# Optimization experiments

Hardware: AMD Instinct MI355X
Metric: run time of the kernel (lower is better)

Reference implementation:

```python
import jax, jax.numpy as jnp
import numpy as np

N, C, H, W = 32, 256, 64, 64
K = 1024  # embed_size


def setup_inputs() -> dict:
    key = jax.random.key(0)
    k1, k2 = jax.random.split(key)
    x = jax.random.normal(k1, (N, C, H, W), dtype=jnp.float32)
    embed = jax.random.normal(k2, (K, C), dtype=jnp.float32)  # codebook buffer
    return {"x": x, "embed": embed}


def reference(x, embed):
    n, c, h, w = x.shape
    # [N,C,H,W] -> [N*H*W, C]
    flat = jnp.transpose(x, (0, 2, 3, 1)).reshape(-1, c)
    # squared euclidean distance; sqrt omitted since argmin is invariant
    d = (
        jnp.sum(flat * flat, axis=-1, keepdims=True)
        - 2.0 * flat @ embed.T
        + jnp.sum(embed * embed, axis=-1)
    )  # [N*H*W, K]
    embed_idx = jnp.argmin(d, axis=1).reshape(n, h, w)
    quantize = embed[embed_idx]  # [N,H,W,C]
    quantize = jnp.transpose(quantize, (0, 3, 1, 2))  # [N,C,H,W]
    diff = jnp.mean((jax.lax.stop_gradient(quantize) - x) ** 2)
    quantize = x + jax.lax.stop_gradient(quantize - x)  # straight-through
    return quantize, embed_idx, diff
```

## Files before the change

kernel.cpp:

```cpp
#include <hip/hip_runtime.h>

#define NB    32
#define CDIM  256
#define HWSZ  4096
#define NPOS  (NB*HWSZ)
#define KCODES 1024
#define QELEMS ((size_t)NB*CDIM*HWSZ)
#define IDX_OFF QELEMS
#define DIFF_OFF (QELEMS + NPOS)
#define EBYTES (32*32768)
#define E2F_OFF (EBYTES/4)

#define AOFF  0
#define BOFF  65536
#define X2P   131072
#define X2T   133120
#define MVOFF 133376
#define MIOFF 135424
#define LDSSZ 137472

typedef _Float16       f16x8  __attribute__((ext_vector_type(8)));
typedef float          f32x16 __attribute__((ext_vector_type(16)));
typedef unsigned short u16x8  __attribute__((ext_vector_type(8)));

static __device__ inline unsigned short f2h(float f) {
    _Float16 h = (_Float16)f;
    return __builtin_bit_cast(unsigned short, h);
}

__global__ __launch_bounds__(64) void vq_prep_embed(const float* __restrict__ embed,
                                                    float* __restrict__ out) {
    const int k = blockIdx.x;
    const int lane = threadIdx.x;
    const float4 v = *reinterpret_cast<const float4*>(embed + (size_t)k * CDIM + lane * 4);

    unsigned char* __restrict__ ebuf = (unsigned char*)out;

    _Float16 h0 = (_Float16)v.x, h1 = (_Float16)v.y, h2 = (_Float16)v.z, h3 = (_Float16)v.w;
    ushort4 hv = { __builtin_bit_cast(unsigned short, h0), __builtin_bit_cast(unsigned short, h1),
                   __builtin_bit_cast(unsigned short, h2), __builtin_bit_cast(unsigned short, h3) };
    ushort4 lv = { f2h((v.x - (float)h0) * 64.0f), f2h((v.y - (float)h1) * 64.0f),
                   f2h((v.z - (float)h2) * 64.0f), f2h((v.w - (float)h3) * 64.0f) };

    const int c0   = lane * 4;
    const int tile = c0 >> 4;
    const int kh   = (c0 >> 3) & 1;
    const int sub  = c0 & 7;
    const size_t byte = (size_t)tile * 32768 + (size_t)kh * 16384 + (size_t)k * 16 + sub * 2;
    *reinterpret_cast<ushort4*>(ebuf + byte)              = hv;
    *reinterpret_cast<ushort4*>(ebuf + byte + 16 * 32768) = lv;

    float s = v.x * v.x + v.y * v.y + v.z * v.z + v.w * v.w;
    #pragma unroll
    for (int m = 1; m < 64; m <<= 1) s += __shfl_xor(s, m, 64);
    if (lane == 0) out[E2F_OFF + k] = s;
    if (k == 0 && lane == 0) out[DIFF_OFF] = 0.0f;
}

__global__ __launch_bounds__(512, 2) void vq_stage1(const float* __restrict__ x,
                                                    float* __restrict__ out) {
    __shared__ __align__(16) unsigned char lds[LDSSZ];

    const unsigned char* __restrict__ ebuf = (const unsigned char*)out;
    const float* __restrict__ e2buf = out + E2F_OFF;
    float* __restrict__ idx_out = out + IDX_OFF;

    const int t     = threadIdx.x;
    const int lane  = t & 63;
    const int col32 = lane & 31;
    const int hi    = lane >> 5;
    const int widx  = t >> 6;

    const int pos0 = blockIdx.x * 64;
    const int n    = pos0 >> 12;
    const int hw0  = pos0 & 4095;
    const float* __restrict__ xbase = x + (size_t)n * (CDIM * HWSZ) + hw0;

    {
        const int i = t & 63;
        const int g = t >> 6;
        float x2p = 0.f;
        #pragma unroll
        for (int j = 0; j < 4; ++j) {
            const int c0 = g * 32 + j * 8;
            u16x8 hv, lv;
            #pragma unroll
            for (int q = 0; q < 8; ++q) {
                float vv = xbase[(size_t)(c0 + q) * HWSZ + i];
                x2p = fmaf(vv, vv, x2p);
                _Float16 hh = (_Float16)vv;
                hv[q] = __builtin_bit_cast(unsigned short, hh);
                lv[q] = f2h((vv - (float)hh) * 64.0f);
            }
            const int a  = c0 >> 4;
            const int kh = (c0 >> 3) & 1;
            const int byte = a * 2048 + kh * 1024 + i * 16;
            *reinterpret_cast<u16x8*>(lds + byte)         = hv;
            *reinterpret_cast<u16x8*>(lds + byte + 32768) = lv;
        }
        ((float*)(lds + X2P))[g * 64 + i] = x2p;
    }

    auto stage = [&](int tile, int buf) {
        const unsigned char* src = ebuf + (size_t)tile * 32768;
        unsigned char* dst = lds + BOFF + buf * 32768;
        #pragma unroll
        for (int ii = 0; ii < 4; ++ii) {
            const int chunk = (widx * 4 + ii) * 1024;
            __builtin_amdgcn_global_load_lds(
                (const __attribute__((address_space(1))) unsigned int*)(src + chunk + lane * 16),
                (__attribute__((address_space(3))) unsigned int*)(dst + chunk),
                16, 0, 0);
        }
    };

    stage(0, 0);
    __syncthreads();

    if (t < 64) {
        const float* p = (const float*)(lds + X2P);
        float s = 0.f;
        #pragma unroll
        for (int g = 0; g < 8; ++g) s += p[g * 64 + t];
        ((float*)(lds + X2T))[t] = s;
    }

    f32x16 acc[2][4];
    #pragma unroll
    for (int ra = 0; ra < 2; ++ra)
        #pragma unroll
        for (int cb = 0; cb < 4; ++cb)
            #pragma unroll
            for (int r = 0; r < 16; ++r) acc[ra][cb][r] = 0.f;

    const int aoff_lane = hi * 1024 + col32 * 16;
    const int boff_lane = hi * 16384 + (widx * 128 + col32) * 16;

    int buf = 0;
    for (int kq = 0; kq < 48; ++kq) {
        const int nb = kq + 1;
        if (nb < 48) stage(nb < 32 ? nb : nb - 32, buf ^ 1);

        const int a = (kq < 16) ? kq : kq - 16;
        const unsigned char* ab = lds + a * 2048;
        const unsigned char* bb = lds + BOFF + buf * 32768;

        f16x8 av[2], bv[4];
        #pragma unroll
        for (int ra = 0; ra < 2; ++ra)
            av[ra] = *reinterpret_cast<const f16x8*>(ab + aoff_lane + ra * 512);
        #pragma unroll
        for (int cb = 0; cb < 4; ++cb)
            bv[cb] = *reinterpret_cast<const f16x8*>(bb + boff_lane + cb * 512);

        if (kq >= 16 && kq < 32) {
            #pragma unroll
            for (int ra = 0; ra < 2; ++ra) av[ra] *= (_Float16)0.015625f;
        } else if (kq >= 32) {
            #pragma unroll
            for (int cb = 0; cb < 4; ++cb) bv[cb] *= (_Float16)0.015625f;
        }

        __builtin_amdgcn_s_setprio(1);
        #pragma unroll
        for (int ra = 0; ra < 2; ++ra)
            #pragma unroll
            for (int cb = 0; cb < 4; ++cb)
                acc[ra][cb] = __builtin_amdgcn_mfma_f32_32x32x16_f16(
                    av[ra], bv[cb], acc[ra][cb], 0, 0, 0);
        __builtin_amdgcn_s_setprio(0);

        __syncthreads();
        buf ^= 1;
    }

    const float* x2t = (const float*)(lds + X2T);
    float e2v[4];
    #pragma unroll
    for (int cb = 0; cb < 4; ++cb)
        e2v[cb] = e2buf[widx * 128 + cb * 32 + col32];

    float* mv = (float*)(lds + MVOFF);
    int*   mi = (int*)(lds + MIOFF);

    #pragma unroll
    for (int ra = 0; ra < 2; ++ra) {
        #pragma unroll
        for (int reg = 0; reg < 16; ++reg) {
            const int pos = ra * 32 + (reg & 3) + 8 * (reg >> 2) + 4 * hi;
            const float x2 = x2t[pos];
            float bv_ = 3.4e38f;
            int   bi_ = 0;
            #pragma unroll
            for (int cb = 0; cb < 4; ++cb) {
                const int code = widx * 128 + cb * 32 + col32;
                const float s = (x2 - 2.0f * acc[ra][cb][reg]) + e2v[cb];
                if (s < bv_) { bv_ = s; bi_ = code; }
            }
            #pragma unroll
            for (int m = 1; m < 32; m <<= 1) {
                float ov = __shfl_xor(bv_, m, 64);
                int   oi = __shfl_xor(bi_, m, 64);
                if (ov < bv_ || (ov == bv_ && oi < bi_)) { bv_ = ov; bi_ = oi; }
            }
            if (col32 == 0) {
                mv[widx * 64 + pos] = bv_;
                mi[widx * 64 + pos] = bi_;
            }
        }
    }

    __syncthreads();
    if (t < 64) {
        float bv_ = mv[t];
        int   bi_ = mi[t];
        #pragma unroll
        for (int w = 1; w < 8; ++w) {
            const float ov = mv[w * 64 + t];
            const int   oi = mi[w * 64 + t];
            if (ov < bv_ || (ov == bv_ && oi < bi_)) { bv_ = ov; bi_ = oi; }
        }
        idx_out[pos0 + t] = (float)bi_;
        float d = bv_;
        #pragma unroll
        for (int m = 1; m < 64; m <<= 1) d += __shfl_xor(d, m, 64);
        if (t == 0) atomicAdd(out + DIFF_OFF, d * (1.0f / 33554432.0f));
    }
}

__global__ __launch_bounds__(256) void vq_gather_kernel(const float* __restrict__ embed,
                                                        float* __restrict__ out) {
    const int tid = threadIdx.x;
    const int p = blockIdx.x * 256 + tid;
    const int n = p >> 12;
    const int hw = p & 4095;
    const int idx = (int)out[IDX_OFF + p];
    const float4* __restrict__ erow4 = reinterpret_cast<const float4*>(embed + (size_t)idx * CDIM);
    float* __restrict__ op = out + (size_t)n * (CDIM * HWSZ) + hw;

    #pragma unroll 8
    for (int c4 = 0; c4 < 64; ++c4) {
        const float4 e = erow4[c4];
        op[(size_t)(c4 * 4 + 0) * HWSZ] = e.x;
        op[(size_t)(c4 * 4 + 1) * HWSZ] = e.y;
        op[(size_t)(c4 * 4 + 2) * HWSZ] = e.z;
        op[(size_t)(c4 * 4 + 3) * HWSZ] = e.w;
    }
}

extern "C" void kernel_launch(void* const* d_in, const int* in_sizes, int n_in,
                              void* d_out, int out_size, void* d_ws, size_t ws_size,
                              hipStream_t stream) {
    const float* x = (const float*)d_in[0];
    const float* embed = (const float*)d_in[1];
    float* out = (float*)d_out;

    vq_prep_embed<<<KCODES, 64, 0, stream>>>(embed, out);
    vq_stage1<<<NPOS / 64, 512, 0, stream>>>(x, out);
    vq_gather_kernel<<<NPOS / 256, 256, 0, stream>>>(embed, out);
}
```

Baseline: 431.9 us.

## Reuse each staged codebook tile for hi and lo A parts in one pass

The K-loop shrinks from 48 iterations to 32. Each codebook tile is staged once, and while it is resident it is used for both the high and low fp16 split of the activations, where before several tiles were restaged. This cuts global-to-LDS traffic and barrier count. The per-iteration __syncthreads is replaced with an explicit vmcnt wait plus raw s_barrier pairs, so prefetch stays in flight across the barrier. The manual waitcnt accounting is fragile, and the final prefetch wraps to tile 0 and loads data that is never used.

Result: slower. 1.277 ms (+195.7%).

```diff
diff --git a/kernel.cpp b/kernel.cpp
--- a/kernel.cpp
+++ b/kernel.cpp
@@ -11,7 +11,6 @@
 #define EBYTES (32*32768)
 #define E2F_OFF (EBYTES/4)
 
-#define AOFF  0
 #define BOFF  65536
 #define X2P   131072
 #define X2T   133120
@@ -114,8 +113,8 @@
         }
     };
 
+    __syncthreads();
     stage(0, 0);
-    __syncthreads();
 
     if (t < 64) {
         const float* p = (const float*)(lds + X2P);
@@ -136,42 +135,64 @@
     const int aoff_lane = hi * 1024 + col32 * 16;
     const int boff_lane = hi * 16384 + (widx * 128 + col32) * 16;
 
-    int buf = 0;
-    for (int kq = 0; kq < 48; ++kq) {
-        const int nb = kq + 1;
-        if (nb < 48) stage(nb < 32 ? nb : nb - 32, buf ^ 1);
-
-        const int a = (kq < 16) ? kq : kq - 16;
-        const unsigned char* ab = lds + a * 2048;
-        const unsigned char* bb = lds + BOFF + buf * 32768;
-
-        f16x8 av[2], bv[4];
-        #pragma unroll
-        for (int ra = 0; ra < 2; ++ra)
-            av[ra] = *reinterpret_cast<const f16x8*>(ab + aoff_lane + ra * 512);
-        #pragma unroll
-        for (int cb = 0; cb < 4; ++cb)
-            bv[cb] = *reinterpret_cast<const f16x8*>(bb + boff_lane + cb * 512);
-
-        if (kq >= 16 && kq < 32) {
-            #pragma unroll
-            for (int ra = 0; ra < 2; ++ra) av[ra] *= (_Float16)0.015625f;
-        } else if (kq >= 32) {
+    for (int kt = 0; kt < 32; ++kt) {
+        stage((kt + 1) & 31, (kt + 1) & 1);
+        asm volatile("s_waitcnt vmcnt(4)" ::: "memory");
+        __builtin_amdgcn_s_barrier();
+
+        const unsigned char* bb = lds + BOFF + (kt & 1) * 32768;
+
+        if (kt < 16) {
+            const unsigned char* ab = lds + kt * 2048;
+            f16x8 ah[2], al[2], bv[4];
+            #pragma unroll
+            for (int ra = 0; ra < 2; ++ra) {
+                ah[ra] = *reinterpret_cast<const f16x8*>(ab + aoff_lane + ra * 512);
+                al[ra] = *reinterpret_cast<const f16x8*>(ab + 32768 + aoff_lane + ra * 512);
+            }
+            #pragma unroll
+            for (int cb = 0; cb < 4; ++cb)
+                bv[cb] = *reinterpret_cast<const f16x8*>(bb + boff_lane + cb * 512);
+
+            __builtin_amdgcn_s_setprio(1);
+            #pragma unroll
+            for (int ra = 0; ra < 2; ++ra)
+                #pragma unroll
+                for (int cb = 0; cb < 4; ++cb)
+                    acc[ra][cb] = __builtin_amdgcn_mfma_f32_32x32x16_f16(
+                        ah[ra], bv[cb], acc[ra][cb], 0, 0, 0);
             #pragma unroll
             for (int cb = 0; cb < 4; ++cb) bv[cb] *= (_Float16)0.015625f;
-        }
-
-        __builtin_amdgcn_s_setprio(1);
-        #pragma unroll
-        for (int ra = 0; ra < 2; ++ra)
+            #pragma unroll
+            for (int ra = 0; ra < 2; ++ra)
+                #pragma unroll
+                for (int cb = 0; cb < 4; ++cb)
+                    acc[ra][cb] = __builtin_amdgcn_mfma_f32_32x32x16_f16(
+                        al[ra], bv[cb], acc[ra][cb], 0, 0, 0);
+            __builtin_amdgcn_s_setprio(0);
+        } else {
+            const unsigned char* ab = lds + (kt - 16) * 2048;
+            f16x8 ah[2], bv[4];
+            #pragma unroll
+            for (int ra = 0; ra < 2; ++ra) {
+                ah[ra] = *reinterpret_cast<const f16x8*>(ab + aoff_lane + ra * 512);
+                ah[ra] *= (_Float16)0.015625f;
+            }
             #pragma unroll
             for (int cb = 0; cb < 4; ++cb)
-                acc[ra][cb] = __builtin_amdgcn_mfma_f32_32x32x16_f16(
-                    av[ra], bv[cb], acc[ra][cb], 0, 0, 0);
-        __builtin_amdgcn_s_setprio(0);
-
-        __syncthreads();
-        buf ^= 1;
+                bv[cb] = *reinterpret_cast<const f16x8*>(bb + boff_lane + cb * 512);
+
+            __builtin_amdgcn_s_setprio(1);
+            #pragma unroll
+            for (int ra = 0; ra < 2; ++ra)
+                #pragma unroll
+                for (int cb = 0; cb < 4; ++cb)
+                    acc[ra][cb] = __builtin_amdgcn_mfma_f32_32x32x16_f16(
+                        ah[ra], bv[cb], acc[ra][cb], 0, 0, 0);
+            __builtin_amdgcn_s_setprio(0);
+        }
+
+        __builtin_amdgcn_s_barrier();
     }
 
     const float* x2t = (const float*)(lds + X2T);
```

## Load codebook fragments straight from global memory instead of LDS double buffering

Applied to the files above, without the earlier changes.

The per-iteration global_load_lds staging of codebook tiles into double-buffered LDS is removed. Each wave now reads its own 128-code B fragments directly from global memory (L2) into registers, using a re-laid-out prepped codebook where each code row is 32 contiguous bytes. Because each wave only ever consumed its own slice of the staged tile, the staging added no reuse. Dropping it removes the per-iteration __syncthreads and roughly halves LDS use, which may allow more resident blocks per CU. In exchange, global-memory latency is exposed in the MFMA loop, covered only by a 2x unroll and whatever occupancy is gained.

After: 413.3 us. 4.3% less time.

```diff
diff --git a/kernel.cpp b/kernel.cpp
--- a/kernel.cpp
+++ b/kernel.cpp
@@ -11,13 +11,11 @@
 #define EBYTES (32*32768)
 #define E2F_OFF (EBYTES/4)
 
-#define AOFF  0
-#define BOFF  65536
-#define X2P   131072
-#define X2T   133120
-#define MVOFF 133376
-#define MIOFF 135424
-#define LDSSZ 137472
+#define X2P   65536
+#define X2T   67584
+#define MVOFF 67840
+#define MIOFF 69888
+#define LDSSZ 71936
 
 typedef _Float16       f16x8  __attribute__((ext_vector_type(8)));
 typedef float          f32x16 __attribute__((ext_vector_type(16)));
@@ -42,11 +40,11 @@
     ushort4 lv = { f2h((v.x - (float)h0) * 64.0f), f2h((v.y - (float)h1) * 64.0f),
                    f2h((v.z - (float)h2) * 64.0f), f2h((v.w - (float)h3) * 64.0f) };
 
-    const int c0   = lane * 4;
-    const int tile = c0 >> 4;
-    const int kh   = (c0 >> 3) & 1;
-    const int sub  = c0 & 7;
-    const size_t byte = (size_t)tile * 32768 + (size_t)kh * 16384 + (size_t)k * 16 + sub * 2;
+    const int c0  = lane * 4;
+    const int r   = c0 >> 4;
+    const int hi  = (c0 >> 3) & 1;
+    const int sub = c0 & 7;
+    const size_t byte = (size_t)r * 32768 + (size_t)k * 32 + hi * 16 + sub * 2;
     *reinterpret_cast<ushort4*>(ebuf + byte)              = hv;
     *reinterpret_cast<ushort4*>(ebuf + byte + 16 * 32768) = lv;
 
@@ -57,8 +55,8 @@
     if (k == 0 && lane == 0) out[DIFF_OFF] = 0.0f;
 }
 
-__global__ __launch_bounds__(512, 2) void vq_stage1(const float* __restrict__ x,
-                                                    float* __restrict__ out) {
+__global__ __launch_bounds__(512) void vq_stage1(const float* __restrict__ x,
+                                                 float* __restrict__ out) {
     __shared__ __align__(16) unsigned char lds[LDSSZ];
 
     const unsigned char* __restrict__ ebuf = (const unsigned char*)out;
@@ -92,29 +90,14 @@
                 hv[q] = __builtin_bit_cast(unsigned short, hh);
                 lv[q] = f2h((vv - (float)hh) * 64.0f);
             }
-            const int a  = c0 >> 4;
+            const int kc = c0 >> 4;
             const int kh = (c0 >> 3) & 1;
-            const int byte = a * 2048 + kh * 1024 + i * 16;
+            const int byte = kc * 2048 + kh * 1024 + i * 16;
             *reinterpret_cast<u16x8*>(lds + byte)         = hv;
             *reinterpret_cast<u16x8*>(lds + byte + 32768) = lv;
         }
         ((float*)(lds + X2P))[g * 64 + i] = x2p;
     }
-
-    auto stage = [&](int tile, int buf) {
-        const unsigned char* src = ebuf + (size_t)tile * 32768;
-        unsigned char* dst = lds + BOFF + buf * 32768;
-        #pragma unroll
-        for (int ii = 0; ii < 4; ++ii) {
-            const int chunk = (widx * 4 + ii) * 1024;
-            __builtin_amdgcn_global_load_lds(
-                (const __attribute__((address_space(1))) unsigned int*)(src + chunk + lane * 16),
-                (__attribute__((address_space(3))) unsigned int*)(dst + chunk),
-                16, 0, 0);
-        }
-    };
-
-    stage(0, 0);
     __syncthreads();
 
     if (t < 64) {
@@ -124,6 +107,7 @@
         for (int g = 0; g < 8; ++g) s += p[g * 64 + t];
         ((float*)(lds + X2T))[t] = s;
     }
+    __syncthreads();
 
     f32x16 acc[2][4];
     #pragma unroll
@@ -133,45 +117,44 @@
             #pragma unroll
             for (int r = 0; r < 16; ++r) acc[ra][cb][r] = 0.f;
 
-    const int aoff_lane = hi * 1024 + col32 * 16;
-    const int boff_lane = hi * 16384 + (widx * 128 + col32) * 16;
-
-    int buf = 0;
+    const int aoff = hi * 1024 + col32 * 16;
+    const unsigned char* __restrict__ bbase =
+        ebuf + (size_t)widx * 4096 + (size_t)col32 * 32 + (size_t)hi * 16;
+
+    #pragma unroll 2
     for (int kq = 0; kq < 48; ++kq) {
-        const int nb = kq + 1;
-        if (nb < 48) stage(nb < 32 ? nb : nb - 32, buf ^ 1);
-
-        const int a = (kq < 16) ? kq : kq - 16;
-        const unsigned char* ab = lds + a * 2048;
-        const unsigned char* bb = lds + BOFF + buf * 32768;
-
-        f16x8 av[2], bv[4];
-        #pragma unroll
-        for (int ra = 0; ra < 2; ++ra)
-            av[ra] = *reinterpret_cast<const f16x8*>(ab + aoff_lane + ra * 512);
-        #pragma unroll
-        for (int cb = 0; cb < 4; ++cb)
-            bv[cb] = *reinterpret_cast<const f16x8*>(bb + boff_lane + cb * 512);
-
-        if (kq >= 16 && kq < 32) {
-            #pragma unroll
-            for (int ra = 0; ra < 2; ++ra) av[ra] *= (_Float16)0.015625f;
-        } else if (kq >= 32) {
-            #pragma unroll
-            for (int cb = 0; cb < 4; ++cb) bv[cb] *= (_Float16)0.015625f;
+        const int seg = kq >> 4;
+        const int r   = (kq < 32) ? kq : (kq - 32);
+        const unsigned char* ab = lds + (kq & 15) * 2048 + ((seg == 2) ? 32768 : 0);
+        const unsigned char* bp = bbase + (size_t)r * 32768;
+
+        f16x8 a0 = *reinterpret_cast<const f16x8*>(ab + aoff);
+        f16x8 a1 = *reinterpret_cast<const f16x8*>(ab + aoff + 512);
+        f16x8 b0 = *reinterpret_cast<const f16x8*>(bp);
+        f16x8 b1 = *reinterpret_cast<const f16x8*>(bp + 1024);
+        f16x8 b2 = *reinterpret_cast<const f16x8*>(bp + 2048);
+        f16x8 b3 = *reinterpret_cast<const f16x8*>(bp + 3072);
+
+        if (seg == 1) {
+            a0 *= (_Float16)0.015625f;
+            a1 *= (_Float16)0.015625f;
+        } else if (seg == 2) {
+            b0 *= (_Float16)0.015625f;
+            b1 *= (_Float16)0.015625f;
+            b2 *= (_Float16)0.015625f;
+            b3 *= (_Float16)0.015625f;
         }
 
         __builtin_amdgcn_s_setprio(1);
-        #pragma unroll
-        for (int ra = 0; ra < 2; ++ra)
-            #pragma unroll
-            for (int cb = 0; cb < 4; ++cb)
-                acc[ra][cb] = __builtin_amdgcn_mfma_f32_32x32x16_f16(
-                    av[ra], bv[cb], acc[ra][cb], 0, 0, 0);
+        acc[0][0] = __builtin_amdgcn_mfma_f32_32x32x16_f16(a0, b0, acc[0][0], 0, 0, 0);
+        acc[0][1] = __builtin_amdgcn_mfma_f32_32x32x16_f16(a0, b1, acc[0][1], 0, 0, 0);
+        acc[0][2] = __builtin_amdgcn_mfma_f32_32x32x16_f16(a0, b2, acc[0][2], 0, 0, 0);
+        acc[0][3] = __builtin_amdgcn_mfma_f32_32x32x16_f16(a0, b3, acc[0][3], 0, 0, 0);
+        acc[1][0] = __builtin_amdgcn_mfma_f32_32x32x16_f16(a1, b0, acc[1][0], 0, 0, 0);
+        acc[1][1] = __builtin_amdgcn_mfma_f32_32x32x16_f16(a1, b1, acc[1][1], 0, 0, 0);
+        acc[1][2] = __builtin_amdgcn_mfma_f32_32x32x16_f16(a1, b2, acc[1][2], 0, 0, 0);
+        acc[1][3] = __builtin_amdgcn_mfma_f32_32x32x16_f16(a1, b3, acc[1][3], 0, 0, 0);
         __builtin_amdgcn_s_setprio(0);
-
-        __syncthreads();
-        buf ^= 1;
     }
 
     const float* x2t = (const float*)(lds + X2T);
```
